# Performance work log

Hardware: AMD Instinct MI355X
Metric: run time of the kernel (lower is better)

## Reference

```python
import jax, jax.numpy as jnp
import numpy as np

GRID = 1024   # grid side -> V = GRID^2 verts
BATCH = 8     # homogeneous batch of meshes


def _grid_mesh_faces(S):
    # Triangulated regular grid: 2 triangles per cell.
    idx = np.arange(S * S, dtype=np.int64).reshape(S, S)
    a = idx[:-1, :-1].ravel()
    b = a + 1
    c = a + S
    d = a + S + 1
    f1 = np.stack([a, b, c], axis=1)
    f2 = np.stack([b, d, c], axis=1)
    return np.concatenate([f1, f2], axis=0)  # (F, 3) int64


def _unique_edges(faces, V):
    # Edge k of a face is opposite vertex k (pytorch3d convention):
    # edges = [(v1,v2), (v0,v2), (v0,v1)]
    e = np.stack([faces[:, [1, 2]], faces[:, [0, 2]], faces[:, [0, 1]]], axis=1)  # (F,3,2)
    e = np.sort(e, axis=-1)
    keys = e[..., 0] * np.int64(V) + e[..., 1]
    uniq, inv = np.unique(keys.ravel(), return_inverse=True)
    edges = np.stack([uniq // V, uniq % V], axis=1).astype(np.int64)  # (E,2)
    face_to_edge = inv.reshape(-1, 3).astype(np.int64)                # (F,3)
    return edges, face_to_edge


def setup_inputs() -> dict:
    key = jax.random.key(0)
    V = GRID * GRID
    faces_np = _grid_mesh_faces(GRID)
    edges_np, fte_np = _unique_edges(faces_np, V)
    verts = jax.random.normal(key, (BATCH, V, 3), dtype=jnp.float32)
    return {
        "verts": verts,
        "faces": jnp.asarray(faces_np),
        "edges": jnp.asarray(edges_np),
        "face_to_edge": jnp.asarray(fte_np),
    }


def reference(verts, faces, edges, face_to_edge):
    # verts: (N, V, 3); faces: (F, 3); edges: (E, 2); face_to_edge: (F, 3)
    N, V, _ = verts.shape
    # Gather edge endpoints and average to midpoints: (N, E, 2, 3) -> (N, E, 3)
    mid = verts[:, edges].mean(axis=2)
    # New verts = original verts followed by edge midpoints
    new_verts = jnp.concatenate([verts, mid], axis=1)  # (N, V+E, 3)
    # New faces (pytorch3d SubdivideMeshes._subdivide_faces ordering):
    e = face_to_edge + V  # midpoint vertex indices
    f0 = jnp.stack([faces[:, 0], e[:, 2], e[:, 1]], axis=1)
    f1 = jnp.stack([faces[:, 1], e[:, 0], e[:, 2]], axis=1)
    f2 = jnp.stack([faces[:, 2], e[:, 1], e[:, 0]], axis=1)
    f3 = e
    new_faces = jnp.concatenate([f0, f1, f2, f3], axis=0)  # (4F, 3)
    return new_verts, new_faces
```

## Files before the change

### kernel.cpp

```cpp
#include <hip/hip_runtime.h>


#define GRID_S 1024
#define V_CONST (GRID_S * GRID_S)

__global__ void copy_verts_k(const float* __restrict__ verts,
                             float* __restrict__ out,
                             int perBatch,
                             int rowStride3,
                             int total) {
    int i = blockIdx.x * blockDim.x + threadIdx.x;
    if (i >= total) return;
    int n = i / perBatch;
    int r = i - n * perBatch;
    out[n * rowStride3 + r] = verts[i];
}

__global__ void midpoints_k(const float* __restrict__ verts,
                            const int* __restrict__ edges,
                            float* __restrict__ out,
                            int E,
                            int rowStride3) {
    int e = blockIdx.x * blockDim.x + threadIdx.x;
    if (e >= E) return;
    int n = blockIdx.y;
    int v0 = edges[2 * e];
    int v1 = edges[2 * e + 1];
    const float* b = verts + n * (V_CONST * 3);
    float x = 0.5f * (b[3 * v0 + 0] + b[3 * v1 + 0]);
    float y = 0.5f * (b[3 * v0 + 1] + b[3 * v1 + 1]);
    float z = 0.5f * (b[3 * v0 + 2] + b[3 * v1 + 2]);
    int o = n * rowStride3 + (V_CONST + e) * 3;
    out[o + 0] = x;
    out[o + 1] = y;
    out[o + 2] = z;
}

__global__ void faces_k(const int* __restrict__ faces,
                        const int* __restrict__ fte,
                        float* __restrict__ out,
                        int F,
                        int baseOut) {
    int f = blockIdx.x * blockDim.x + threadIdx.x;
    if (f >= F) return;
    int a = faces[3 * f + 0];
    int b = faces[3 * f + 1];
    int c = faces[3 * f + 2];
    int e0 = fte[3 * f + 0] + V_CONST;
    int e1 = fte[3 * f + 1] + V_CONST;
    int e2 = fte[3 * f + 2] + V_CONST;
    float* o0 = out + baseOut + 3 * f;
    float* o1 = o0 + 3 * F;
    float* o2 = o1 + 3 * F;
    float* o3 = o2 + 3 * F;
    o0[0] = (float)a;  o0[1] = (float)e2; o0[2] = (float)e1;
    o1[0] = (float)b;  o1[1] = (float)e0; o1[2] = (float)e2;
    o2[0] = (float)c;  o2[1] = (float)e1; o2[2] = (float)e0;
    o3[0] = (float)e0; o3[1] = (float)e1; o3[2] = (float)e2;
}

extern "C" void kernel_launch(void* const* d_in, const int* in_sizes, int n_in,
                              void* d_out, int out_size, void* d_ws, size_t ws_size,
                              hipStream_t stream) {
    const float* verts = (const float*)d_in[0];
    const int* faces   = (const int*)d_in[1];
    const int* edges   = (const int*)d_in[2];
    const int* fte     = (const int*)d_in[3];
    float* out = (float*)d_out;

    const int F = in_sizes[1] / 3;
    const int E = in_sizes[2] / 2;
    const int N = in_sizes[0] / (V_CONST * 3);

    const int perBatch   = V_CONST * 3;
    const int rowStride3 = (V_CONST + E) * 3;
    const int totalCopy  = N * perBatch;
    const int baseOut    = N * rowStride3;

    {
        int threads = 256;
        int blocks = (totalCopy + threads - 1) / threads;
        copy_verts_k<<<blocks, threads, 0, stream>>>(verts, out, perBatch,
                                                     rowStride3, totalCopy);
    }
    {
        dim3 block(256);
        dim3 grid((E + 255) / 256, N);
        midpoints_k<<<grid, block, 0, stream>>>(verts, edges, out, E, rowStride3);
    }
    {
        int threads = 256;
        int blocks = (F + threads - 1) / threads;
        faces_k<<<blocks, threads, 0, stream>>>(faces, fte, out, F, baseOut);
    }
}
```

Baseline: 690.7 us.

## Map threads to output components for coalesced stores in all three kernels

Each kernel now assigns one thread per output float instead of one thread per vertex, edge or face. The midpoint and face kernels previously wrote strided 3- or 12-float records per thread, and now every warp writes a contiguous range. The vertex copy uses a 2D grid to avoid a per-element integer division, and offsets use 64-bit arithmetic. The cost is redundant reads of edge and face index data, plus extra divide-by-3 and branch work per thread.

```diff
diff --git a/kernel.cpp b/kernel.cpp
--- a/kernel.cpp
+++ b/kernel.cpp
@@ -3,60 +3,57 @@
 
 #define GRID_S 1024
 #define V_CONST (GRID_S * GRID_S)
+#define V3_CONST (V_CONST * 3)
 
-__global__ void copy_verts_k(const float* __restrict__ verts,
-                             float* __restrict__ out,
-                             int perBatch,
-                             int rowStride3,
-                             int total) {
-    int i = blockIdx.x * blockDim.x + threadIdx.x;
-    if (i >= total) return;
-    int n = i / perBatch;
-    int r = i - n * perBatch;
-    out[n * rowStride3 + r] = verts[i];
+__global__ __launch_bounds__(256) void copy_verts_k(
+    const float* __restrict__ verts,
+    float* __restrict__ out,
+    int rowStride3) {
+    int r = blockIdx.x * blockDim.x + threadIdx.x;
+    if (r >= V3_CONST) return;
+    int n = blockIdx.y;
+    out[(long)n * rowStride3 + r] = verts[(long)n * V3_CONST + r];
 }
 
-__global__ void midpoints_k(const float* __restrict__ verts,
-                            const int* __restrict__ edges,
-                            float* __restrict__ out,
-                            int E,
-                            int rowStride3) {
-    int e = blockIdx.x * blockDim.x + threadIdx.x;
-    if (e >= E) return;
+__global__ __launch_bounds__(256) void midpoints_k(
+    const float* __restrict__ verts,
+    const int* __restrict__ edges,
+    float* __restrict__ out,
+    int E3,
+    int rowStride3) {
+    int rem = blockIdx.x * blockDim.x + threadIdx.x;
+    if (rem >= E3) return;
     int n = blockIdx.y;
+    int e = rem / 3;
+    int c = rem - 3 * e;
     int v0 = edges[2 * e];
     int v1 = edges[2 * e + 1];
-    const float* b = verts + n * (V_CONST * 3);
-    float x = 0.5f * (b[3 * v0 + 0] + b[3 * v1 + 0]);
-    float y = 0.5f * (b[3 * v0 + 1] + b[3 * v1 + 1]);
-    float z = 0.5f * (b[3 * v0 + 2] + b[3 * v1 + 2]);
-    int o = n * rowStride3 + (V_CONST + e) * 3;
-    out[o + 0] = x;
-    out[o + 1] = y;
-    out[o + 2] = z;
+    const float* b = verts + (long)n * V3_CONST;
+    float val = 0.5f * (b[3 * v0 + c] + b[3 * v1 + c]);
+    out[(long)n * rowStride3 + V3_CONST + rem] = val;
 }
 
-__global__ void faces_k(const int* __restrict__ faces,
-                        const int* __restrict__ fte,
-                        float* __restrict__ out,
-                        int F,
-                        int baseOut) {
-    int f = blockIdx.x * blockDim.x + threadIdx.x;
-    if (f >= F) return;
-    int a = faces[3 * f + 0];
-    int b = faces[3 * f + 1];
-    int c = faces[3 * f + 2];
-    int e0 = fte[3 * f + 0] + V_CONST;
-    int e1 = fte[3 * f + 1] + V_CONST;
-    int e2 = fte[3 * f + 2] + V_CONST;
-    float* o0 = out + baseOut + 3 * f;
-    float* o1 = o0 + 3 * F;
-    float* o2 = o1 + 3 * F;
-    float* o3 = o2 + 3 * F;
-    o0[0] = (float)a;  o0[1] = (float)e2; o0[2] = (float)e1;
-    o1[0] = (float)b;  o1[1] = (float)e0; o1[2] = (float)e2;
-    o2[0] = (float)c;  o2[1] = (float)e1; o2[2] = (float)e0;
-    o3[0] = (float)e0; o3[1] = (float)e1; o3[2] = (float)e2;
+__global__ __launch_bounds__(256) void faces_k(
+    const int* __restrict__ faces,
+    const int* __restrict__ fte,
+    float* __restrict__ out,
+    int threeF,
+    long baseOut) {
+    int t = blockIdx.x * blockDim.x + threadIdx.x;
+    if (t >= threeF) return;
+    int r = blockIdx.y;
+    int f = t / 3;
+    int k = t - 3 * f;
+    int val;
+    if (r == 3) {
+        val = fte[t] + V_CONST;
+    } else if (k == 0) {
+        val = faces[3 * f + r];
+    } else {
+        int idx = (k == 1) ? (r + 2) % 3 : (r + 1) % 3;
+        val = fte[3 * f + idx] + V_CONST;
+    }
+    out[baseOut + (long)r * threeF + t] = (float)val;
 }
 
 extern "C" void kernel_launch(void* const* d_in, const int* in_sizes, int n_in,
@@ -70,27 +67,26 @@
 
     const int F = in_sizes[1] / 3;
     const int E = in_sizes[2] / 2;
-    const int N = in_sizes[0] / (V_CONST * 3);
+    const int N = in_sizes[0] / V3_CONST;
 
-    const int perBatch   = V_CONST * 3;
     const int rowStride3 = (V_CONST + E) * 3;
-    const int totalCopy  = N * perBatch;
-    const int baseOut    = N * rowStride3;
+    const int E3 = E * 3;
+    const int threeF = 3 * F;
+    const long baseOut = (long)N * rowStride3;
 
     {
-        int threads = 256;
-        int blocks = (totalCopy + threads - 1) / threads;
-        copy_verts_k<<<blocks, threads, 0, stream>>>(verts, out, perBatch,
-                                                     rowStride3, totalCopy);
+        dim3 block(256);
+        dim3 grid((V3_CONST + 255) / 256, N);
+        copy_verts_k<<<grid, block, 0, stream>>>(verts, out, rowStride3);
     }
     {
         dim3 block(256);
-        dim3 grid((E + 255) / 256, N);
-        midpoints_k<<<grid, block, 0, stream>>>(verts, edges, out, E, rowStride3);
+        dim3 grid((E3 + 255) / 256, N);
+        midpoints_k<<<grid, block, 0, stream>>>(verts, edges, out, E3, rowStride3);
     }
     {
-        int threads = 256;
-        int blocks = (F + threads - 1) / threads;
-        faces_k<<<blocks, threads, 0, stream>>>(faces, fte, out, F, baseOut);
+        dim3 block(256);
+        dim3 grid((threeF + 255) / 256, 4);
+        faces_k<<<grid, block, 0, stream>>>(faces, fte, out, threeF, baseOut);
     }
 }
```

New measurement: 845.1 us. +22.4%, slower.
